# Performance work log

Hardware: AMD Instinct MI355X
Metric: run time of the kernel (lower is better)

Reference implementation:

```python
import jax, jax.numpy as jnp
import numpy as np

HIDDEN = 128
IN = 2
OUT = 2

def setup_inputs() -> dict:
    key = jax.random.key(0)
    ks = jax.random.split(key, 12)
    B, S = 1024, 512
    s_ih = 1.0 / np.sqrt(HIDDEN)
    return {
        "x0": jax.random.normal(ks[0], (B, OUT), jnp.float32),
        "v_seq": jax.random.normal(ks[1], (B, S, IN), jnp.float32),
        # GRU params (PyTorch layout: gates ordered r, z, n)
        "W_ih": jax.random.uniform(ks[2], (3 * HIDDEN, IN), jnp.float32, -s_ih, s_ih),
        "W_hh": jax.random.uniform(ks[3], (3 * HIDDEN, HIDDEN), jnp.float32, -s_ih, s_ih),
        "b_ih": jax.random.uniform(ks[4], (3 * HIDDEN,), jnp.float32, -s_ih, s_ih),
        "b_hh": jax.random.uniform(ks[5], (3 * HIDDEN,), jnp.float32, -s_ih, s_ih),
        # output Linear hidden -> OUT
        "W_out": jax.random.uniform(ks[6], (OUT, HIDDEN), jnp.float32, -s_ih, s_ih),
        "b_out": jax.random.uniform(ks[7], (OUT,), jnp.float32, -s_ih, s_ih),
        # residual predictor: Linear(OUT+IN -> HIDDEN//2), ReLU, Linear(-> OUT)
        "W_r1": jax.random.uniform(ks[8], (HIDDEN // 2, OUT + IN), jnp.float32, -0.5, 0.5),
        "b_r1": jax.random.uniform(ks[9], (HIDDEN // 2,), jnp.float32, -0.5, 0.5),
        "W_r2": jax.random.uniform(ks[10], (OUT, HIDDEN // 2), jnp.float32, -s_ih, s_ih),
        "b_r2": jax.random.uniform(ks[11], (OUT,), jnp.float32, -s_ih, s_ih),
    }

def _gru_seq(v_seq, W_ih, W_hh, b_ih, b_hh):
    B, S, _ = v_seq.shape
    H = W_hh.shape[1]
    # precompute input projections for all timesteps: [B,S,3H]
    xp = jnp.einsum('bsi,gi->bsg', v_seq, W_ih) + b_ih
    xp = jnp.swapaxes(xp, 0, 1)  # [S,B,3H]

    def step(h, xp_t):
        gh = h @ W_hh.T + b_hh  # [B,3H]
        xr, xz, xn = jnp.split(xp_t, 3, axis=-1)
        hr, hz, hn = jnp.split(gh, 3, axis=-1)
        r = jax.nn.sigmoid(xr + hr)
        z = jax.nn.sigmoid(xz + hz)
        n = jnp.tanh(xn + r * hn)
        h_new = (1.0 - z) * n + z * h
        return h_new, h_new

    h0 = jnp.zeros((B, H), v_seq.dtype)
    _, h_seq = jax.lax.scan(step, h0, xp)
    return jnp.swapaxes(h_seq, 0, 1)  # [B,S,H]

def reference(x0, v_seq, W_ih, W_hh, b_ih, b_hh, W_out, b_out, W_r1, b_r1, W_r2, b_r2):
    h_seq = _gru_seq(v_seq, W_ih, W_hh, b_ih, b_hh)
    x_pred = jnp.einsum('bsh,oh->bso', h_seq, W_out) + b_out  # [B,S,OUT]
    # In the torch loop, x_prev at step t is x0 for t=0 else x_pred[:,t-1],
    # so the loop vectorizes as a shift along time.
    x_prev = jnp.concatenate([x0[:, None, :], x_pred[:, :-1, :]], axis=1)
    # input_size == output_size, so v_t[:, :OUT] == v_t (no padding branch)
    ri = jnp.concatenate([x_prev, v_seq], axis=-1)  # [B,S,OUT+IN]
    hid = jax.nn.relu(jnp.einsum('bsf,hf->bsh', ri, W_r1) + b_r1)
    residual = jnp.einsum('bsh,oh->bso', hid, W_r2) + b_r2
    physics_pred = x_prev + v_seq + residual
    physics_violations = x_pred - physics_pred
    return (x_pred, physics_violations)
```

## Files before the change

### kernel.cpp

```cpp
#include <hip/hip_runtime.h>
#include <stdint.h>

#define BB 1024
#define SS 512
#define HH 128
#define MM 4
#define BLK 512
#define NBLK (BB / MM)
#define RS 32
#define RStr 136

typedef float f32x4 __attribute__((ext_vector_type(4)));
typedef float f32x2 __attribute__((ext_vector_type(2)));
typedef _Float16 f16x8 __attribute__((ext_vector_type(8)));

#define LO_SCALE 2048.0f
#define LO_INV   (1.0f / 2048.0f)
#define L2E      1.44269504088896f

__device__ __forceinline__ float rcp_fast(float x)  { return __builtin_amdgcn_rcpf(x); }
__device__ __forceinline__ float exp2_fast(float x) { return __builtin_amdgcn_exp2f(x); }

__global__ __launch_bounds__(BLK, 2) void pig_kernel(
    const float* __restrict__ x0, const float* __restrict__ v_seq,
    const float* __restrict__ W_ih, const float* __restrict__ W_hh,
    const float* __restrict__ b_ih, const float* __restrict__ b_hh,
    const float* __restrict__ W_out, const float* __restrict__ b_out,
    const float* __restrict__ W_r1, const float* __restrict__ b_r1,
    const float* __restrict__ W_r2, const float* __restrict__ b_r2,
    float* __restrict__ out)
{
    __shared__ __align__(16) _Float16 hp2[2][1024];
    __shared__ __align__(16) _Float16 ring[RS * 4 * RStr];
    __shared__ __align__(16) float    v_lds[SS * 8];
    __shared__ __align__(16) float    xs[RS + 1][8];
    __shared__ __align__(16) float    wpk[64][8];
    __shared__ float xc[2][8];

    const int tid  = threadIdx.x;
    const int wave = tid >> 6;
    const int lane = tid & 63;
    const int quad = lane >> 4;
    const int col  = lane & 15;
    const int row0 = blockIdx.x * MM;
    const int j    = wave * 16 + col;

    f16x8 whi[3][4];
#pragma unroll
    for (int nt = 0; nt < 3; ++nt) {
        const int g = nt * HH + j;
#pragma unroll
        for (int kk = 0; kk < 4; ++kk) {
            const float* p = W_hh + g * HH + kk * 32 + quad * 8;
            f16x8 fh;
#pragma unroll
            for (int i = 0; i < 8; ++i) fh[i] = (_Float16)p[i];
            whi[nt][kk] = fh;
        }
    }

    const float wr0 = W_ih[j*2],        wr1 = W_ih[j*2+1];
    const float wz0 = W_ih[(HH+j)*2],   wz1 = W_ih[(HH+j)*2+1];
    const float wn0 = W_ih[(2*HH+j)*2], wn1 = W_ih[(2*HH+j)*2+1];
    const float br  = b_ih[j]      + b_hh[j];
    const float bz  = b_ih[HH+j]   + b_hh[HH+j];
    const float bni = b_ih[2*HH+j];
    const float bnh = b_hh[2*HH+j];

    const int rr    = ((col >> 2) << 1) | (col & 1);
    const int rbase = quad * 64 + rr * 8;
    const int wbase = ((j >> 5) << 8) + (((j >> 3) & 3) << 6) + (quad << 4) + (j & 7);

    const int g8  = tid >> 3;
    const int l8  = tid & 7;
    const int oA  = g8 & 1;
    const int mA  = (g8 >> 1) & 3;
    const int tt8 = g8 >> 3;
    float woA[16];
#pragma unroll
    for (int i = 0; i < 16; ++i) woA[i] = W_out[oA * HH + l8 * 16 + i];
    const float boA = b_out[oA];

    const int qB = tid & 3;
    const int mB = (tid >> 2) & 3;
    const int tB = tid >> 4;
    const float b2B = b_r2[qB & 1];

    for (int idx = tid; idx < 2 * 1024; idx += BLK) ((_Float16*)hp2)[idx] = (_Float16)0.0f;
    for (int idx = tid; idx < MM * SS * 2; idx += BLK) {
        const int m = idx >> 10, i = idx & 1023;
        v_lds[(i >> 1) * 8 + m * 2 + (i & 1)] = v_seq[(size_t)(row0 + m) * (SS * 2) + i];
    }
    if (tid < 64) {
        wpk[tid][0] = W_r1[tid*4];   wpk[tid][1] = W_r1[tid*4+1];
        wpk[tid][2] = W_r1[tid*4+2]; wpk[tid][3] = W_r1[tid*4+3];
        wpk[tid][4] = b_r1[tid];
        wpk[tid][5] = W_r2[tid];     wpk[tid][6] = W_r2[64 + tid];
        wpk[tid][7] = 0.0f;
    }
    if (tid < 8)
        xc[0][tid] = x0[(size_t)(row0 + (tid >> 1)) * 2 + (tid & 1)];
    __syncthreads();

    float hold = 0.0f;
    f32x2 vv2 = *(const f32x2*)&v_lds[quad * 2];

    for (int t = 0; t < SS; ++t) {
        const int cur = t & 1, nxt = cur ^ 1;

        f32x4 aH0 = {0,0,0,0}, aH1 = {0,0,0,0}, aH2 = {0,0,0,0};
        const _Float16* hb = &hp2[cur][rbase];
#pragma unroll
        for (int kk = 0; kk < 4; ++kk) {
            f16x8 af = *(const f16x8*)&hb[kk * 256];
            aH0 = __builtin_amdgcn_mfma_f32_16x16x32_f16(af, whi[0][kk], aH0, 0, 0, 0);
            aH1 = __builtin_amdgcn_mfma_f32_16x16x32_f16(af, whi[1][kk], aH1, 0, 0, 0);
            aH2 = __builtin_amdgcn_mfma_f32_16x16x32_f16(af, whi[2][kk], aH2, 0, 0, 0);
        }
        const float gh0 = fmaf(aH0[1], LO_INV, aH0[0]);
        const float gh1 = fmaf(aH1[1], LO_INV, aH1[0]);
        const float gh2 = fmaf(aH2[1], LO_INV, aH2[0]);

        const float ra = gh0 + vv2[0]*wr0 + vv2[1]*wr1 + br;
        const float r  = rcp_fast(1.0f + exp2_fast(ra * (-L2E)));
        const float za = gh1 + vv2[0]*wz0 + vv2[1]*wz1 + bz;
        const float z  = rcp_fast(1.0f + exp2_fast(za * (-L2E)));
        const float na = vv2[0]*wn0 + vv2[1]*wn1 + bni + r * (gh2 + bnh);
        const float n  = fmaf(2.0f, rcp_fast(1.0f + exp2_fast(na * (-2.0f * L2E))), -1.0f);
        hold = fmaf(z, hold - n, n);

        const _Float16 hh = (_Float16)hold;
        hp2[nxt][wbase]     = hh;
        hp2[nxt][wbase + 8] = (_Float16)((hold - (float)hh) * LO_SCALE);
        ring[((t & (RS-1)) * 4 + quad) * RStr + j] = hh;

        vv2 = *(const f32x2*)&v_lds[((t + 1) & (SS - 1)) * 8 + quad * 2];

        __syncthreads();

        if ((t & (RS - 1)) == (RS - 1)) {
            const int f  = t >> 5;
            const int t0 = t - (RS - 1);

            if (tid < 8) xs[0][tid] = xc[f & 1][tid];
#pragma unroll
            for (int p = 0; p < 4; ++p) {
                const int tt = p * 8 + tt8;
                const f16x8 h0 = *(const f16x8*)&ring[(tt * 4 + mA) * RStr + l8 * 16];
                const f16x8 h1 = *(const f16x8*)&ring[(tt * 4 + mA) * RStr + l8 * 16 + 8];
                float acc = 0.0f;
#pragma unroll
                for (int i = 0; i < 8; ++i) {
                    acc += (float)h0[i] * woA[i];
                    acc += (float)h1[i] * woA[8 + i];
                }
                acc += __shfl_xor(acc, 1, 64);
                acc += __shfl_xor(acc, 2, 64);
                acc += __shfl_xor(acc, 4, 64);
                if (l8 == 0) xs[1 + tt][mA * 2 + oA] = acc + boA;
            }
            __syncthreads();

            {
                const float xp0 = xs[tB][mB*2], xp1 = xs[tB][mB*2+1];
                const f32x2 vt2 = *(const f32x2*)&v_lds[(t0 + tB) * 8 + mB * 2];
                float rss0 = 0.0f, rss1 = 0.0f;
#pragma unroll
                for (int uu = 0; uu < 16; ++uu) {
                    const int u = qB * 16 + uu;
                    const f32x4 wA = *(const f32x4*)&wpk[u][0];
                    const f32x4 wB = *(const f32x4*)&wpk[u][4];
                    const float hu = fmaxf(wB[0] + wA[0]*xp0 + wA[1]*xp1 + wA[2]*vt2[0] + wA[3]*vt2[1], 0.0f);
                    rss0 += hu * wB[1];
                    rss1 += hu * wB[2];
                }
                rss0 += __shfl_xor(rss0, 1, 64);
                rss1 += __shfl_xor(rss1, 1, 64);
                rss0 += __shfl_xor(rss0, 2, 64);
                rss1 += __shfl_xor(rss1, 2, 64);
                if (qB < 2) {
                    const int o = qB;
                    const float xpred = xs[tB + 1][mB*2 + o];
                    const float xpv   = xs[tB][mB*2 + o];
                    const float vv    = v_lds[(t0 + tB) * 8 + mB*2 + o];
                    const float resid = (o ? rss1 : rss0) + b2B;
                    const float viol  = xpred - (xpv + vv + resid);
                    const size_t base = (size_t)(row0 + mB) * (SS * 2) + (t0 + tB) * 2 + o;
                    out[base] = xpred;
                    out[(size_t)BB * SS * 2 + base] = viol;
                }
                if (tid < 8) xc[(f + 1) & 1][tid] = xs[RS][tid];
            }
            __syncthreads();
        }
    }
}

extern "C" void kernel_launch(void* const* d_in, const int* in_sizes, int n_in,
                              void* d_out, int out_size, void* d_ws, size_t ws_size,
                              hipStream_t stream) {
    pig_kernel<<<dim3(NBLK), dim3(BLK), 0, stream>>>(
        (const float*)d_in[0],  (const float*)d_in[1],  (const float*)d_in[2],
        (const float*)d_in[3],  (const float*)d_in[4],  (const float*)d_in[5],
        (const float*)d_in[6],  (const float*)d_in[7],  (const float*)d_in[8],
        (const float*)d_in[9],  (const float*)d_in[10], (const float*)d_in[11],
        (float*)d_out);
}
```

Measured before the change: 343.6 us.

## Halve batch rows per block and remap waves to cover two gate column tiles

Each block now handles 2 batch rows with 256 threads (4 waves) instead of 4 rows with 512 threads, giving 512 blocks. Each wave issues MFMAs for two 16-column tiles and picks its own result lanes with selects. The hi/lo fp16 split packs the hidden state into the A operand differently. The aim is more blocks across CUs and cheaper per-step barriers with fewer waves, at the cost of twice the MFMA count per wave, more weight registers, and wasted MFMA rows.

```diff
diff --git a/kernel.cpp b/kernel.cpp
--- a/kernel.cpp
+++ b/kernel.cpp
@@ -4,8 +4,8 @@
 #define BB 1024
 #define SS 512
 #define HH 128
-#define MM 4
-#define BLK 512
+#define MM 2
+#define BLK 256
 #define NBLK (BB / MM)
 #define RS 32
 #define RStr 136
@@ -30,12 +30,12 @@
     const float* __restrict__ W_r2, const float* __restrict__ b_r2,
     float* __restrict__ out)
 {
-    __shared__ __align__(16) _Float16 hp2[2][1024];
-    __shared__ __align__(16) _Float16 ring[RS * 4 * RStr];
-    __shared__ __align__(16) float    v_lds[SS * 8];
-    __shared__ __align__(16) float    xs[RS + 1][8];
+    __shared__ __align__(16) _Float16 hp2[2][512];
+    __shared__ __align__(16) _Float16 ring[RS * 2 * RStr];
+    __shared__ __align__(16) float    v_lds[SS * 4];
+    __shared__ __align__(16) float    xs[RS + 1][4];
     __shared__ __align__(16) float    wpk[64][8];
-    __shared__ float xc[2][8];
+    __shared__ float xc[2][4];
 
     const int tid  = threadIdx.x;
     const int wave = tid >> 6;
@@ -43,19 +43,24 @@
     const int quad = lane >> 4;
     const int col  = lane & 15;
     const int row0 = blockIdx.x * MM;
-    const int j    = wave * 16 + col;
-
-    f16x8 whi[3][4];
+    const int ct   = quad & 1;
+    const int mq   = quad >> 1;
+    const int j    = wave * 32 + ct * 16 + col;
+
+    f16x8 whi[3][4][2];
 #pragma unroll
     for (int nt = 0; nt < 3; ++nt) {
-        const int g = nt * HH + j;
-#pragma unroll
-        for (int kk = 0; kk < 4; ++kk) {
-            const float* p = W_hh + g * HH + kk * 32 + quad * 8;
-            f16x8 fh;
-#pragma unroll
-            for (int i = 0; i < 8; ++i) fh[i] = (_Float16)p[i];
-            whi[nt][kk] = fh;
+#pragma unroll
+        for (int c = 0; c < 2; ++c) {
+            const int g = nt * HH + wave * 32 + c * 16 + col;
+#pragma unroll
+            for (int kk = 0; kk < 4; ++kk) {
+                const float* p = W_hh + g * HH + kk * 32 + quad * 8;
+                f16x8 fh;
+#pragma unroll
+                for (int i = 0; i < 8; ++i) fh[i] = (_Float16)p[i];
+                whi[nt][kk][c] = fh;
+            }
         }
     }
 
@@ -67,29 +72,28 @@
     const float bni = b_ih[2*HH+j];
     const float bnh = b_hh[2*HH+j];
 
-    const int rr    = ((col >> 2) << 1) | (col & 1);
-    const int rbase = quad * 64 + rr * 8;
-    const int wbase = ((j >> 5) << 8) + (((j >> 3) & 3) << 6) + (quad << 4) + (j & 7);
+    const int rbase = quad * 32 + (col & 3) * 8;
+    const int wbase = wave * 128 + ((j >> 3) & 3) * 32 + mq * 16 + (j & 7);
 
     const int g8  = tid >> 3;
     const int l8  = tid & 7;
     const int oA  = g8 & 1;
-    const int mA  = (g8 >> 1) & 3;
-    const int tt8 = g8 >> 3;
+    const int mA  = (g8 >> 1) & 1;
+    const int tt8 = g8 >> 2;
     float woA[16];
 #pragma unroll
     for (int i = 0; i < 16; ++i) woA[i] = W_out[oA * HH + l8 * 16 + i];
     const float boA = b_out[oA];
 
     const int qB = tid & 3;
-    const int mB = (tid >> 2) & 3;
-    const int tB = tid >> 4;
+    const int mB = (tid >> 2) & 1;
+    const int tB = tid >> 3;
     const float b2B = b_r2[qB & 1];
 
-    for (int idx = tid; idx < 2 * 1024; idx += BLK) ((_Float16*)hp2)[idx] = (_Float16)0.0f;
+    for (int idx = tid; idx < 2 * 512; idx += BLK) ((_Float16*)hp2)[idx] = (_Float16)0.0f;
     for (int idx = tid; idx < MM * SS * 2; idx += BLK) {
         const int m = idx >> 10, i = idx & 1023;
-        v_lds[(i >> 1) * 8 + m * 2 + (i & 1)] = v_seq[(size_t)(row0 + m) * (SS * 2) + i];
+        v_lds[(i >> 1) * 4 + m * 2 + (i & 1)] = v_seq[(size_t)(row0 + m) * (SS * 2) + i];
     }
     if (tid < 64) {
         wpk[tid][0] = W_r1[tid*4];   wpk[tid][1] = W_r1[tid*4+1];
@@ -98,28 +102,45 @@
         wpk[tid][5] = W_r2[tid];     wpk[tid][6] = W_r2[64 + tid];
         wpk[tid][7] = 0.0f;
     }
-    if (tid < 8)
+    if (tid < 4)
         xc[0][tid] = x0[(size_t)(row0 + (tid >> 1)) * 2 + (tid & 1)];
     __syncthreads();
 
     float hold = 0.0f;
-    f32x2 vv2 = *(const f32x2*)&v_lds[quad * 2];
+    f32x2 vv2 = *(const f32x2*)&v_lds[mq * 2];
 
     for (int t = 0; t < SS; ++t) {
         const int cur = t & 1, nxt = cur ^ 1;
 
-        f32x4 aH0 = {0,0,0,0}, aH1 = {0,0,0,0}, aH2 = {0,0,0,0};
+        f32x4 a0c0 = {0,0,0,0}, a0c1 = {0,0,0,0};
+        f32x4 a1c0 = {0,0,0,0}, a1c1 = {0,0,0,0};
+        f32x4 a2c0 = {0,0,0,0}, a2c1 = {0,0,0,0};
         const _Float16* hb = &hp2[cur][rbase];
 #pragma unroll
         for (int kk = 0; kk < 4; ++kk) {
-            f16x8 af = *(const f16x8*)&hb[kk * 256];
-            aH0 = __builtin_amdgcn_mfma_f32_16x16x32_f16(af, whi[0][kk], aH0, 0, 0, 0);
-            aH1 = __builtin_amdgcn_mfma_f32_16x16x32_f16(af, whi[1][kk], aH1, 0, 0, 0);
-            aH2 = __builtin_amdgcn_mfma_f32_16x16x32_f16(af, whi[2][kk], aH2, 0, 0, 0);
+            f16x8 af = *(const f16x8*)&hb[kk * 128];
+            a0c0 = __builtin_amdgcn_mfma_f32_16x16x32_f16(af, whi[0][kk][0], a0c0, 0, 0, 0);
+            a0c1 = __builtin_amdgcn_mfma_f32_16x16x32_f16(af, whi[0][kk][1], a0c1, 0, 0, 0);
+            a1c0 = __builtin_amdgcn_mfma_f32_16x16x32_f16(af, whi[1][kk][0], a1c0, 0, 0, 0);
+            a1c1 = __builtin_amdgcn_mfma_f32_16x16x32_f16(af, whi[1][kk][1], a1c1, 0, 0, 0);
+            a2c0 = __builtin_amdgcn_mfma_f32_16x16x32_f16(af, whi[2][kk][0], a2c0, 0, 0, 0);
+            a2c1 = __builtin_amdgcn_mfma_f32_16x16x32_f16(af, whi[2][kk][1], a2c1, 0, 0, 0);
         }
-        const float gh0 = fmaf(aH0[1], LO_INV, aH0[0]);
-        const float gh1 = fmaf(aH1[1], LO_INV, aH1[0]);
-        const float gh2 = fmaf(aH2[1], LO_INV, aH2[0]);
+        const float g0A = fmaf(a0c0[1], LO_INV, a0c0[0]);
+        const float g0B = fmaf(a0c0[3], LO_INV, a0c0[2]);
+        const float g0C = fmaf(a0c1[1], LO_INV, a0c1[0]);
+        const float g0D = fmaf(a0c1[3], LO_INV, a0c1[2]);
+        const float gh0 = ct ? (mq ? g0D : g0C) : (mq ? g0B : g0A);
+        const float g1A = fmaf(a1c0[1], LO_INV, a1c0[0]);
+        const float g1B = fmaf(a1c0[3], LO_INV, a1c0[2]);
+        const float g1C = fmaf(a1c1[1], LO_INV, a1c1[0]);
+        const float g1D = fmaf(a1c1[3], LO_INV, a1c1[2]);
+        const float gh1 = ct ? (mq ? g1D : g1C) : (mq ? g1B : g1A);
+        const float g2A = fmaf(a2c0[1], LO_INV, a2c0[0]);
+        const float g2B = fmaf(a2c0[3], LO_INV, a2c0[2]);
+        const float g2C = fmaf(a2c1[1], LO_INV, a2c1[0]);
+        const float g2D = fmaf(a2c1[3], LO_INV, a2c1[2]);
+        const float gh2 = ct ? (mq ? g2D : g2C) : (mq ? g2B : g2A);
 
         const float ra = gh0 + vv2[0]*wr0 + vv2[1]*wr1 + br;
         const float r  = rcp_fast(1.0f + exp2_fast(ra * (-L2E)));
@@ -132,9 +153,9 @@
         const _Float16 hh = (_Float16)hold;
         hp2[nxt][wbase]     = hh;
         hp2[nxt][wbase + 8] = (_Float16)((hold - (float)hh) * LO_SCALE);
-        ring[((t & (RS-1)) * 4 + quad) * RStr + j] = hh;
-
-        vv2 = *(const f32x2*)&v_lds[((t + 1) & (SS - 1)) * 8 + quad * 2];
+        ring[((t & (RS-1)) * 2 + mq) * RStr + j] = hh;
+
+        vv2 = *(const f32x2*)&v_lds[((t + 1) & (SS - 1)) * 4 + mq * 2];
 
         __syncthreads();
 
@@ -142,12 +163,12 @@
             const int f  = t >> 5;
             const int t0 = t - (RS - 1);
 
-            if (tid < 8) xs[0][tid] = xc[f & 1][tid];
+            if (tid < 4) xs[0][tid] = xc[f & 1][tid];
 #pragma unroll
             for (int p = 0; p < 4; ++p) {
                 const int tt = p * 8 + tt8;
-                const f16x8 h0 = *(const f16x8*)&ring[(tt * 4 + mA) * RStr + l8 * 16];
-                const f16x8 h1 = *(const f16x8*)&ring[(tt * 4 + mA) * RStr + l8 * 16 + 8];
+                const f16x8 h0 = *(const f16x8*)&ring[(tt * 2 + mA) * RStr + l8 * 16];
+                const f16x8 h1 = *(const f16x8*)&ring[(tt * 2 + mA) * RStr + l8 * 16 + 8];
                 float acc = 0.0f;
 #pragma unroll
                 for (int i = 0; i < 8; ++i) {
@@ -163,7 +184,7 @@
 
             {
                 const float xp0 = xs[tB][mB*2], xp1 = xs[tB][mB*2+1];
-                const f32x2 vt2 = *(const f32x2*)&v_lds[(t0 + tB) * 8 + mB * 2];
+                const f32x2 vt2 = *(const f32x2*)&v_lds[(t0 + tB) * 4 + mB * 2];
                 float rss0 = 0.0f, rss1 = 0.0f;
 #pragma unroll
                 for (int uu = 0; uu < 16; ++uu) {
@@ -182,14 +203,14 @@
                     const int o = qB;
                     const float xpred = xs[tB + 1][mB*2 + o];
                     const float xpv   = xs[tB][mB*2 + o];
-                    const float vv    = v_lds[(t0 + tB) * 8 + mB*2 + o];
+                    const float vv    = v_lds[(t0 + tB) * 4 + mB*2 + o];
                     const float resid = (o ? rss1 : rss0) + b2B;
                     const float viol  = xpred - (xpv + vv + resid);
                     const size_t base = (size_t)(row0 + mB) * (SS * 2) + (t0 + tB) * 2 + o;
                     out[base] = xpred;
                     out[(size_t)BB * SS * 2 + base] = viol;
                 }
-                if (tid < 8) xc[(f + 1) & 1][tid] = xs[RS][tid];
+                if (tid < 4) xc[(f + 1) & 1][tid] = xs[RS][tid];
             }
             __syncthreads();
         }
```

New measurement: 385.7 us. +12.3%, slower.

## Halve block size so each wave computes two hidden-column tiles

Applied to the files above, without the earlier changes.

Cuts the block from 512 to 256 threads. Each wave now holds W_hh fragments for 32 hidden columns and issues twice as many MFMAs per step, and each thread updates two batch rows' hidden state from the extra accumulator lanes. The aim is cheaper per-step __syncthreads across fewer waves and more MFMA work per wave on the serial recurrence critical path. In exchange, register pressure doubles for the weight fragments and occupancy is reduced to one block per launch bound. The epilogue loops are adjusted to cover the same work with half the threads.

```diff
diff --git a/kernel.cpp b/kernel.cpp
--- a/kernel.cpp
+++ b/kernel.cpp
@@ -5,7 +5,7 @@
 #define SS 512
 #define HH 128
 #define MM 4
-#define BLK 512
+#define BLK 256
 #define NBLK (BB / MM)
 #define RS 32
 #define RStr 136
@@ -21,7 +21,7 @@
 __device__ __forceinline__ float rcp_fast(float x)  { return __builtin_amdgcn_rcpf(x); }
 __device__ __forceinline__ float exp2_fast(float x) { return __builtin_amdgcn_exp2f(x); }
 
-__global__ __launch_bounds__(BLK, 2) void pig_kernel(
+__global__ __launch_bounds__(BLK, 1) void pig_kernel(
     const float* __restrict__ x0, const float* __restrict__ v_seq,
     const float* __restrict__ W_ih, const float* __restrict__ W_hh,
     const float* __restrict__ b_ih, const float* __restrict__ b_hh,
@@ -43,19 +43,24 @@
     const int quad = lane >> 4;
     const int col  = lane & 15;
     const int row0 = blockIdx.x * MM;
-    const int j    = wave * 16 + col;
-
-    f16x8 whi[3][4];
+    const int cthi = quad >> 1;
+    const int ma   = (quad & 1) * 2;
+    const int j    = wave * 32 + cthi * 16 + col;
+
+    f16x8 whi[3][4][2];
 #pragma unroll
     for (int nt = 0; nt < 3; ++nt) {
-        const int g = nt * HH + j;
-#pragma unroll
-        for (int kk = 0; kk < 4; ++kk) {
-            const float* p = W_hh + g * HH + kk * 32 + quad * 8;
-            f16x8 fh;
-#pragma unroll
-            for (int i = 0; i < 8; ++i) fh[i] = (_Float16)p[i];
-            whi[nt][kk] = fh;
+#pragma unroll
+        for (int c = 0; c < 2; ++c) {
+            const int g = nt * HH + wave * 32 + c * 16 + col;
+#pragma unroll
+            for (int kk = 0; kk < 4; ++kk) {
+                const float* p = W_hh + g * HH + kk * 32 + quad * 8;
+                f16x8 fh;
+#pragma unroll
+                for (int i = 0; i < 8; ++i) fh[i] = (_Float16)p[i];
+                whi[nt][kk][c] = fh;
+            }
         }
     }
 
@@ -67,9 +72,8 @@
     const float bni = b_ih[2*HH+j];
     const float bnh = b_hh[2*HH+j];
 
-    const int rr    = ((col >> 2) << 1) | (col & 1);
-    const int rbase = quad * 64 + rr * 8;
-    const int wbase = ((j >> 5) << 8) + (((j >> 3) & 3) << 6) + (quad << 4) + (j & 7);
+    const int rbase = quad * 64 + (col & 7) * 8;
+    const int wbase = (j >> 5) * 256 + ((j >> 3) & 3) * 64 + (quad & 1) * 32 + (j & 7);
 
     const int g8  = tid >> 3;
     const int l8  = tid & 7;
@@ -81,9 +85,9 @@
     for (int i = 0; i < 16; ++i) woA[i] = W_out[oA * HH + l8 * 16 + i];
     const float boA = b_out[oA];
 
-    const int qB = tid & 3;
-    const int mB = (tid >> 2) & 3;
-    const int tB = tid >> 4;
+    const int qB  = tid & 3;
+    const int mB  = (tid >> 2) & 3;
+    const int tB4 = tid >> 4;
     const float b2B = b_r2[qB & 1];
 
     for (int idx = tid; idx < 2 * 1024; idx += BLK) ((_Float16*)hp2)[idx] = (_Float16)0.0f;
@@ -102,39 +106,63 @@
         xc[0][tid] = x0[(size_t)(row0 + (tid >> 1)) * 2 + (tid & 1)];
     __syncthreads();
 
-    float hold = 0.0f;
-    f32x2 vv2 = *(const f32x2*)&v_lds[quad * 2];
+    float hold0 = 0.0f, hold1 = 0.0f;
+    f32x4 vv4 = *(const f32x4*)&v_lds[(quad & 1) * 4];
 
     for (int t = 0; t < SS; ++t) {
         const int cur = t & 1, nxt = cur ^ 1;
 
-        f32x4 aH0 = {0,0,0,0}, aH1 = {0,0,0,0}, aH2 = {0,0,0,0};
+        f32x4 a0c0 = {0,0,0,0}, a0c1 = {0,0,0,0};
+        f32x4 a1c0 = {0,0,0,0}, a1c1 = {0,0,0,0};
+        f32x4 a2c0 = {0,0,0,0}, a2c1 = {0,0,0,0};
         const _Float16* hb = &hp2[cur][rbase];
 #pragma unroll
         for (int kk = 0; kk < 4; ++kk) {
             f16x8 af = *(const f16x8*)&hb[kk * 256];
-            aH0 = __builtin_amdgcn_mfma_f32_16x16x32_f16(af, whi[0][kk], aH0, 0, 0, 0);
-            aH1 = __builtin_amdgcn_mfma_f32_16x16x32_f16(af, whi[1][kk], aH1, 0, 0, 0);
-            aH2 = __builtin_amdgcn_mfma_f32_16x16x32_f16(af, whi[2][kk], aH2, 0, 0, 0);
+            a0c0 = __builtin_amdgcn_mfma_f32_16x16x32_f16(af, whi[0][kk][0], a0c0, 0, 0, 0);
+            a0c1 = __builtin_amdgcn_mfma_f32_16x16x32_f16(af, whi[0][kk][1], a0c1, 0, 0, 0);
+            a1c0 = __builtin_amdgcn_mfma_f32_16x16x32_f16(af, whi[1][kk][0], a1c0, 0, 0, 0);
+            a1c1 = __builtin_amdgcn_mfma_f32_16x16x32_f16(af, whi[1][kk][1], a1c1, 0, 0, 0);
+            a2c0 = __builtin_amdgcn_mfma_f32_16x16x32_f16(af, whi[2][kk][0], a2c0, 0, 0, 0);
+            a2c1 = __builtin_amdgcn_mfma_f32_16x16x32_f16(af, whi[2][kk][1], a2c1, 0, 0, 0);
         }
-        const float gh0 = fmaf(aH0[1], LO_INV, aH0[0]);
-        const float gh1 = fmaf(aH1[1], LO_INV, aH1[0]);
-        const float gh2 = fmaf(aH2[1], LO_INV, aH2[0]);
-
-        const float ra = gh0 + vv2[0]*wr0 + vv2[1]*wr1 + br;
-        const float r  = rcp_fast(1.0f + exp2_fast(ra * (-L2E)));
-        const float za = gh1 + vv2[0]*wz0 + vv2[1]*wz1 + bz;
-        const float z  = rcp_fast(1.0f + exp2_fast(za * (-L2E)));
-        const float na = vv2[0]*wn0 + vv2[1]*wn1 + bni + r * (gh2 + bnh);
-        const float n  = fmaf(2.0f, rcp_fast(1.0f + exp2_fast(na * (-2.0f * L2E))), -1.0f);
-        hold = fmaf(z, hold - n, n);
-
-        const _Float16 hh = (_Float16)hold;
-        hp2[nxt][wbase]     = hh;
-        hp2[nxt][wbase + 8] = (_Float16)((hold - (float)hh) * LO_SCALE);
-        ring[((t & (RS-1)) * 4 + quad) * RStr + j] = hh;
-
-        vv2 = *(const f32x2*)&v_lds[((t + 1) & (SS - 1)) * 8 + quad * 2];
+        const f32x4 A0 = cthi ? a0c1 : a0c0;
+        const f32x4 A1 = cthi ? a1c1 : a1c0;
+        const f32x4 A2 = cthi ? a2c1 : a2c0;
+
+        const float gh0a = fmaf(A0[1], LO_INV, A0[0]);
+        const float gh1a = fmaf(A1[1], LO_INV, A1[0]);
+        const float gh2a = fmaf(A2[1], LO_INV, A2[0]);
+        const float gh0b = fmaf(A0[3], LO_INV, A0[2]);
+        const float gh1b = fmaf(A1[3], LO_INV, A1[2]);
+        const float gh2b = fmaf(A2[3], LO_INV, A2[2]);
+
+        const float raa = gh0a + vv4[0]*wr0 + vv4[1]*wr1 + br;
+        const float ra_ = rcp_fast(1.0f + exp2_fast(raa * (-L2E)));
+        const float zaa = gh1a + vv4[0]*wz0 + vv4[1]*wz1 + bz;
+        const float za_ = rcp_fast(1.0f + exp2_fast(zaa * (-L2E)));
+        const float naa = vv4[0]*wn0 + vv4[1]*wn1 + bni + ra_ * (gh2a + bnh);
+        const float na_ = fmaf(2.0f, rcp_fast(1.0f + exp2_fast(naa * (-2.0f * L2E))), -1.0f);
+        hold0 = fmaf(za_, hold0 - na_, na_);
+
+        const float rab = gh0b + vv4[2]*wr0 + vv4[3]*wr1 + br;
+        const float rb_ = rcp_fast(1.0f + exp2_fast(rab * (-L2E)));
+        const float zab = gh1b + vv4[2]*wz0 + vv4[3]*wz1 + bz;
+        const float zb_ = rcp_fast(1.0f + exp2_fast(zab * (-L2E)));
+        const float nab = vv4[2]*wn0 + vv4[3]*wn1 + bni + rb_ * (gh2b + bnh);
+        const float nb_ = fmaf(2.0f, rcp_fast(1.0f + exp2_fast(nab * (-2.0f * L2E))), -1.0f);
+        hold1 = fmaf(zb_, hold1 - nb_, nb_);
+
+        const _Float16 hh0 = (_Float16)hold0;
+        const _Float16 hh1 = (_Float16)hold1;
+        hp2[nxt][wbase]      = hh0;
+        hp2[nxt][wbase + 8]  = (_Float16)((hold0 - (float)hh0) * LO_SCALE);
+        hp2[nxt][wbase + 16] = hh1;
+        hp2[nxt][wbase + 24] = (_Float16)((hold1 - (float)hh1) * LO_SCALE);
+        ring[((t & (RS-1)) * 4 + ma)     * RStr + j] = hh0;
+        ring[((t & (RS-1)) * 4 + ma + 1) * RStr + j] = hh1;
+
+        vv4 = *(const f32x4*)&v_lds[((t + 1) & (SS - 1)) * 8 + (quad & 1) * 4];
 
         __syncthreads();
 
@@ -144,8 +172,8 @@
 
             if (tid < 8) xs[0][tid] = xc[f & 1][tid];
 #pragma unroll
-            for (int p = 0; p < 4; ++p) {
-                const int tt = p * 8 + tt8;
+            for (int p = 0; p < 8; ++p) {
+                const int tt = p * 4 + tt8;
                 const f16x8 h0 = *(const f16x8*)&ring[(tt * 4 + mA) * RStr + l8 * 16];
                 const f16x8 h1 = *(const f16x8*)&ring[(tt * 4 + mA) * RStr + l8 * 16 + 8];
                 float acc = 0.0f;
@@ -161,7 +189,9 @@
             }
             __syncthreads();
 
-            {
+#pragma unroll
+            for (int c2 = 0; c2 < 2; ++c2) {
+                const int tB = c2 * 16 + tB4;
                 const float xp0 = xs[tB][mB*2], xp1 = xs[tB][mB*2+1];
                 const f32x2 vt2 = *(const f32x2*)&v_lds[(t0 + tB) * 8 + mB * 2];
                 float rss0 = 0.0f, rss1 = 0.0f;
@@ -189,8 +219,8 @@
                     out[base] = xpred;
                     out[(size_t)BB * SS * 2 + base] = viol;
                 }
-                if (tid < 8) xc[(f + 1) & 1][tid] = xs[RS][tid];
             }
+            if (tid < 8) xc[(f + 1) & 1][tid] = xs[RS][tid];
             __syncthreads();
         }
     }
```

Result: slower. 415.4 us (+20.9%).

## Fuse output projection into recurrent MFMA and drop the hidden-state ring buffer

Applied to the files above, without the earlier changes.

Computes the W_out projection of the previous step's hidden state with an extra MFMA that reuses the A fragments already loaded for the recurrent gate product. The per-step x_pred values go straight into xs, so the f16 ring buffer and the periodic scalar dot-product pass over it are removed, and each 32-step flush needs one fewer barrier. The input projection for the next step is also computed ahead of the barrier. In exchange every wave runs an extra MFMA per k-slice on the serial critical path.

```diff
diff --git a/kernel.cpp b/kernel.cpp
--- a/kernel.cpp
+++ b/kernel.cpp
@@ -8,7 +8,6 @@
 #define BLK 512
 #define NBLK (BB / MM)
 #define RS 32
-#define RStr 136
 
 typedef float f32x4 __attribute__((ext_vector_type(4)));
 typedef float f32x2 __attribute__((ext_vector_type(2)));
@@ -31,11 +30,9 @@
     float* __restrict__ out)
 {
     __shared__ __align__(16) _Float16 hp2[2][1024];
-    __shared__ __align__(16) _Float16 ring[RS * 4 * RStr];
     __shared__ __align__(16) float    v_lds[SS * 8];
     __shared__ __align__(16) float    xs[RS + 1][8];
     __shared__ __align__(16) float    wpk[64][8];
-    __shared__ float xc[2][8];
 
     const int tid  = threadIdx.x;
     const int wave = tid >> 6;
@@ -59,6 +56,18 @@
         }
     }
 
+    f16x8 wxo[4];
+    const int oX = col & 1;
+#pragma unroll
+    for (int kk = 0; kk < 4; ++kk) {
+        const float* p = W_out + oX * HH + kk * 32 + quad * 8;
+        f16x8 fh;
+#pragma unroll
+        for (int i = 0; i < 8; ++i) fh[i] = (_Float16)p[i];
+        wxo[kk] = fh;
+    }
+    const float boX = b_out[oX];
+
     const float wr0 = W_ih[j*2],        wr1 = W_ih[j*2+1];
     const float wz0 = W_ih[(HH+j)*2],   wz1 = W_ih[(HH+j)*2+1];
     const float wn0 = W_ih[(2*HH+j)*2], wn1 = W_ih[(2*HH+j)*2+1];
@@ -69,17 +78,7 @@
 
     const int rr    = ((col >> 2) << 1) | (col & 1);
     const int rbase = quad * 64 + rr * 8;
-    const int wbase = ((j >> 5) << 8) + (((j >> 3) & 3) << 6) + (quad << 4) + (j & 7);
-
-    const int g8  = tid >> 3;
-    const int l8  = tid & 7;
-    const int oA  = g8 & 1;
-    const int mA  = (g8 >> 1) & 3;
-    const int tt8 = g8 >> 3;
-    float woA[16];
-#pragma unroll
-    for (int i = 0; i < 16; ++i) woA[i] = W_out[oA * HH + l8 * 16 + i];
-    const float boA = b_out[oA];
+    const int wbase = (j >> 5) * 256 + ((j >> 3) & 3) * 64 + quad * 16 + (j & 7);
 
     const int qB = tid & 3;
     const int mB = (tid >> 2) & 3;
@@ -99,16 +98,49 @@
         wpk[tid][7] = 0.0f;
     }
     if (tid < 8)
-        xc[0][tid] = x0[(size_t)(row0 + (tid >> 1)) * 2 + (tid & 1)];
+        xs[0][tid] = x0[(size_t)(row0 + (tid >> 1)) * 2 + (tid & 1)];
     __syncthreads();
+
+    auto flush = [&](int t0) {
+        const float xp0 = xs[tB][mB*2], xp1 = xs[tB][mB*2+1];
+        const f32x2 vt2 = *(const f32x2*)&v_lds[(t0 + tB) * 8 + mB * 2];
+        float rss0 = 0.0f, rss1 = 0.0f;
+#pragma unroll
+        for (int uu = 0; uu < 16; ++uu) {
+            const int u = qB * 16 + uu;
+            const f32x4 wA = *(const f32x4*)&wpk[u][0];
+            const f32x4 wB = *(const f32x4*)&wpk[u][4];
+            const float hu = fmaxf(wB[0] + wA[0]*xp0 + wA[1]*xp1 + wA[2]*vt2[0] + wA[3]*vt2[1], 0.0f);
+            rss0 += hu * wB[1];
+            rss1 += hu * wB[2];
+        }
+        rss0 += __shfl_xor(rss0, 1, 64);
+        rss1 += __shfl_xor(rss1, 1, 64);
+        rss0 += __shfl_xor(rss0, 2, 64);
+        rss1 += __shfl_xor(rss1, 2, 64);
+        if (qB < 2) {
+            const int o = qB;
+            const float xpred = xs[tB + 1][mB*2 + o];
+            const float xpv   = xs[tB][mB*2 + o];
+            const float vv    = v_lds[(t0 + tB) * 8 + mB*2 + o];
+            const float resid = (o ? rss1 : rss0) + b2B;
+            const float viol  = xpred - (xpv + vv + resid);
+            const size_t base = (size_t)(row0 + mB) * (SS * 2) + (t0 + tB) * 2 + o;
+            out[base] = xpred;
+            out[(size_t)BB * SS * 2 + base] = viol;
+        }
+    };
 
     float hold = 0.0f;
     f32x2 vv2 = *(const f32x2*)&v_lds[quad * 2];
+    float vxr = vv2[0]*wr0 + vv2[1]*wr1 + br;
+    float vxz = vv2[0]*wz0 + vv2[1]*wz1 + bz;
+    float vxn = vv2[0]*wn0 + vv2[1]*wn1 + bni;
 
     for (int t = 0; t < SS; ++t) {
         const int cur = t & 1, nxt = cur ^ 1;
 
-        f32x4 aH0 = {0,0,0,0}, aH1 = {0,0,0,0}, aH2 = {0,0,0,0};
+        f32x4 aH0 = {0,0,0,0}, aH1 = {0,0,0,0}, aH2 = {0,0,0,0}, aX = {0,0,0,0};
         const _Float16* hb = &hp2[cur][rbase];
 #pragma unroll
         for (int kk = 0; kk < 4; ++kk) {
@@ -116,83 +148,51 @@
             aH0 = __builtin_amdgcn_mfma_f32_16x16x32_f16(af, whi[0][kk], aH0, 0, 0, 0);
             aH1 = __builtin_amdgcn_mfma_f32_16x16x32_f16(af, whi[1][kk], aH1, 0, 0, 0);
             aH2 = __builtin_amdgcn_mfma_f32_16x16x32_f16(af, whi[2][kk], aH2, 0, 0, 0);
+            aX  = __builtin_amdgcn_mfma_f32_16x16x32_f16(af, wxo[kk],    aX,  0, 0, 0);
         }
         const float gh0 = fmaf(aH0[1], LO_INV, aH0[0]);
         const float gh1 = fmaf(aH1[1], LO_INV, aH1[0]);
         const float gh2 = fmaf(aH2[1], LO_INV, aH2[0]);
 
-        const float ra = gh0 + vv2[0]*wr0 + vv2[1]*wr1 + br;
-        const float r  = rcp_fast(1.0f + exp2_fast(ra * (-L2E)));
-        const float za = gh1 + vv2[0]*wz0 + vv2[1]*wz1 + bz;
-        const float z  = rcp_fast(1.0f + exp2_fast(za * (-L2E)));
-        const float na = vv2[0]*wn0 + vv2[1]*wn1 + bni + r * (gh2 + bnh);
+        const float r  = rcp_fast(1.0f + exp2_fast((gh0 + vxr) * (-L2E)));
+        const float z  = rcp_fast(1.0f + exp2_fast((gh1 + vxz) * (-L2E)));
+        const float na = vxn + r * (gh2 + bnh);
         const float n  = fmaf(2.0f, rcp_fast(1.0f + exp2_fast(na * (-2.0f * L2E))), -1.0f);
         hold = fmaf(z, hold - n, n);
 
         const _Float16 hh = (_Float16)hold;
         hp2[nxt][wbase]     = hh;
         hp2[nxt][wbase + 8] = (_Float16)((hold - (float)hh) * LO_SCALE);
-        ring[((t & (RS-1)) * 4 + quad) * RStr + j] = hh;
+
+        if (t && tid < 64 && col < 2)
+            xs[1 + ((t - 1) & (RS - 1))][quad * 2 + col] = fmaf(aX[1], LO_INV, aX[0]) + boX;
 
         vv2 = *(const f32x2*)&v_lds[((t + 1) & (SS - 1)) * 8 + quad * 2];
+        vxr = vv2[0]*wr0 + vv2[1]*wr1 + br;
+        vxz = vv2[0]*wz0 + vv2[1]*wz1 + bz;
+        vxn = vv2[0]*wn0 + vv2[1]*wn1 + bni;
 
         __syncthreads();
 
-        if ((t & (RS - 1)) == (RS - 1)) {
-            const int f  = t >> 5;
-            const int t0 = t - (RS - 1);
-
-            if (tid < 8) xs[0][tid] = xc[f & 1][tid];
-#pragma unroll
-            for (int p = 0; p < 4; ++p) {
-                const int tt = p * 8 + tt8;
-                const f16x8 h0 = *(const f16x8*)&ring[(tt * 4 + mA) * RStr + l8 * 16];
-                const f16x8 h1 = *(const f16x8*)&ring[(tt * 4 + mA) * RStr + l8 * 16 + 8];
-                float acc = 0.0f;
-#pragma unroll
-                for (int i = 0; i < 8; ++i) {
-                    acc += (float)h0[i] * woA[i];
-                    acc += (float)h1[i] * woA[8 + i];
-                }
-                acc += __shfl_xor(acc, 1, 64);
-                acc += __shfl_xor(acc, 2, 64);
-                acc += __shfl_xor(acc, 4, 64);
-                if (l8 == 0) xs[1 + tt][mA * 2 + oA] = acc + boA;
-            }
+        if (t && (t & (RS - 1)) == 0) {
+            flush(t - RS);
             __syncthreads();
-
-            {
-                const float xp0 = xs[tB][mB*2], xp1 = xs[tB][mB*2+1];
-                const f32x2 vt2 = *(const f32x2*)&v_lds[(t0 + tB) * 8 + mB * 2];
-                float rss0 = 0.0f, rss1 = 0.0f;
-#pragma unroll
-                for (int uu = 0; uu < 16; ++uu) {
-                    const int u = qB * 16 + uu;
-                    const f32x4 wA = *(const f32x4*)&wpk[u][0];
-                    const f32x4 wB = *(const f32x4*)&wpk[u][4];
-                    const float hu = fmaxf(wB[0] + wA[0]*xp0 + wA[1]*xp1 + wA[2]*vt2[0] + wA[3]*vt2[1], 0.0f);
-                    rss0 += hu * wB[1];
-                    rss1 += hu * wB[2];
-                }
-                rss0 += __shfl_xor(rss0, 1, 64);
-                rss1 += __shfl_xor(rss1, 1, 64);
-                rss0 += __shfl_xor(rss0, 2, 64);
-                rss1 += __shfl_xor(rss1, 2, 64);
-                if (qB < 2) {
-                    const int o = qB;
-                    const float xpred = xs[tB + 1][mB*2 + o];
-                    const float xpv   = xs[tB][mB*2 + o];
-                    const float vv    = v_lds[(t0 + tB) * 8 + mB*2 + o];
-                    const float resid = (o ? rss1 : rss0) + b2B;
-                    const float viol  = xpred - (xpv + vv + resid);
-                    const size_t base = (size_t)(row0 + mB) * (SS * 2) + (t0 + tB) * 2 + o;
-                    out[base] = xpred;
-                    out[(size_t)BB * SS * 2 + base] = viol;
-                }
-                if (tid < 8) xc[(f + 1) & 1][tid] = xs[RS][tid];
-            }
-            __syncthreads();
-        }
+            if (tid < 8) xs[0][tid] = xs[RS][tid];
+        }
+    }
+
+    {
+        f32x4 aX = {0,0,0,0};
+        const _Float16* hb = &hp2[0][rbase];
+#pragma unroll
+        for (int kk = 0; kk < 4; ++kk) {
+            f16x8 af = *(const f16x8*)&hb[kk * 256];
+            aX = __builtin_amdgcn_mfma_f32_16x16x32_f16(af, wxo[kk], aX, 0, 0, 0);
+        }
+        if (tid < 64 && col < 2)
+            xs[RS][quad * 2 + col] = fmaf(aX[1], LO_INV, aX[0]) + boX;
+        __syncthreads();
+        flush(SS - RS);
     }
 }
 
```

After: 362.7 us. 5.6% more time.
